# Optimization experiments

Measured on AMD Instinct MI355X. Metric: run time of the kernel, lower is better.

Reference implementation:

```python
import jax, jax.numpy as jnp
import numpy as np
import math

B, N, C = 2, 2048, 1024
H = 16
D = C // H  # 64


def setup_inputs() -> dict:
    key = jax.random.key(0)
    ks = jax.random.split(key, 11)
    s = 0.02
    return {
        "x": jax.random.normal(ks[0], (B, N, C), jnp.float32),
        "context": jax.random.normal(ks[1], (B, N, C), jnp.float32),
        "attn_bias": jax.random.normal(ks[2], (1, H, N, N), jnp.float32),
        "Wq": jax.random.normal(ks[3], (C, C), jnp.float32) * s,
        "bq": jnp.zeros((C,), jnp.float32),
        "Wk": jax.random.normal(ks[4], (C, C), jnp.float32) * s,
        "bk": jnp.zeros((C,), jnp.float32),
        "Wv": jax.random.normal(ks[5], (C, C), jnp.float32) * s,
        "bv": jnp.zeros((C,), jnp.float32),
        "Wo": jax.random.normal(ks[6], (C, C), jnp.float32) * s,
        "bo": jnp.zeros((C,), jnp.float32),
    }


def reference(x, context, attn_bias, Wq, bq, Wk, bk, Wv, bv, Wo, bo):
    scale = 1.0 / math.sqrt(D)
    # projections (torch Linear: y = x @ W.T + b), reshape to heads
    q = (x @ Wq.T + bq).reshape(B, N, H, D)
    k = (context @ Wk.T + bk).reshape(B, N, H, D)
    v = (context @ Wv.T + bv).reshape(B, N, H, D)
    # scores: (B, H, Nq, Nk)
    sim = jnp.einsum("bqhd,bkhd->bhqk", q, k) * scale + attn_bias
    attn = jax.nn.softmax(sim, axis=-1)
    o = jnp.einsum("bhqk,bkhd->bqhd", attn, v).reshape(B, N, C)
    return o @ Wo.T + bo
```

## Files before the change

### kernel.cpp

```cpp
#include <hip/hip_runtime.h>
#include <stdint.h>
#include <stddef.h>

typedef unsigned short u16;
typedef __attribute__((ext_vector_type(4))) float f32x4;
typedef __attribute__((ext_vector_type(4))) unsigned short u16x4;
typedef __attribute__((ext_vector_type(8))) __bf16 bf16x8;

#define LOG2E 1.44269504088896340736f
#define MSHIFT 23.0831169f

__device__ __forceinline__ u16 f2bf(float f){
  union { float f; uint32_t u; } a; a.f = f;
  uint32_t u = a.u;
  uint32_t r = (u + 0x7FFFu + ((u >> 16) & 1u)) >> 16;
  return (u16)r;
}

__device__ __forceinline__ void gl_lds16(const void* g, void* l){
  __builtin_amdgcn_global_load_lds(
      (const __attribute__((address_space(1))) void*)g,
      (__attribute__((address_space(3))) void*)l,
      16, 0, 0);
}

__global__ __launch_bounds__(256) void cvt6(
    const float* s0, u16* d0, int n0, float f0,
    const float* s1, u16* d1, int n1, float f1,
    const float* s2, u16* d2, int n2, float f2,
    const float* s3, u16* d3, int n3, float f3,
    const float* s4, u16* d4, int n4, float f4,
    const float* s5, u16* d5, int n5, float f5)
{
  const float* s; u16* d; int n; float f;
  switch (blockIdx.y){
    case 0: s=s0; d=d0; n=n0; f=f0; break;
    case 1: s=s1; d=d1; n=n1; f=f1; break;
    case 2: s=s2; d=d2; n=n2; f=f2; break;
    case 3: s=s3; d=d3; n=n3; f=f3; break;
    case 4: s=s4; d=d4; n=n4; f=f4; break;
    default: s=s5; d=d5; n=n5; f=f5; break;
  }
  int tid = blockIdx.x * blockDim.x + threadIdx.x;
  int stride = gridDim.x * blockDim.x;
  for (int i = tid * 4; i < n; i += stride * 4){
    f32x4 v = *(const f32x4*)(s + i);
    u16x4 o;
    o[0] = f2bf(v[0] * f); o[1] = f2bf(v[1] * f);
    o[2] = f2bf(v[2] * f); o[3] = f2bf(v[3] * f);
    *(u16x4*)(d + i) = o;
  }
}

__global__ __launch_bounds__(256, 2) void qkv_gemm(
    const u16* __restrict__ xb, const u16* __restrict__ ctxb,
    const u16* __restrict__ wq, const u16* __restrict__ wkv,
    const float* __restrict__ bq, const float* __restrict__ bk,
    const float* __restrict__ bv,
    u16* __restrict__ q_ws, u16* __restrict__ k_ws, u16* __restrict__ vt_ws)
{
  __shared__ u16 lsA[128 * 64];
  __shared__ u16 lsB[128 * 64];
  const int bid = blockIdx.x;
  const int nb = bid % 24, mb = bid / 24;
  const int tid = threadIdx.x, wave = tid >> 6, lane = tid & 63;
  const int l15 = lane & 15, lg = lane >> 4;
  const int wr = wave >> 1, wc = wave & 1;

  const u16* A; const u16* Bt; const float* bias; int outmode; int nloc;
  float bmul = 1.0f;
  if (nb < 8)      { A = xb;   Bt = wq  + (size_t)(nb * 128) * 1024;            bias = bq; bmul = 0.125f; outmode = 0; nloc = nb; }
  else if (nb < 16){ A = ctxb; Bt = wkv + (size_t)((nb - 8) * 128) * 1024;      bias = bk; outmode = 1; nloc = nb - 8; }
  else             { A = ctxb; Bt = wkv + (size_t)((1024 + (nb - 16) * 128)) * 1024; bias = bv; outmode = 2; nloc = nb - 16; }

  f32x4 acc[4][4] = {};
  const char* Ab = (const char*)(A + (size_t)(mb * 128) * 1024);
  const char* Bb = (const char*)Bt;

  for (int k0 = 0; k0 < 1024; k0 += 64){
    #pragma unroll
    for (int i = 0; i < 4; i++){
      int o = i * 4096 + wave * 1024 + lane * 16;
      int row = o >> 7, cb = o & 127;
      gl_lds16(Ab + (size_t)row * 2048 + (k0 << 1) + cb, (char*)lsA + i * 4096 + wave * 1024);
      gl_lds16(Bb + (size_t)row * 2048 + (k0 << 1) + cb, (char*)lsB + i * 4096 + wave * 1024);
    }
    __syncthreads();
    #pragma unroll
    for (int kk = 0; kk < 2; kk++){
      bf16x8 af[4], bfr[4];
      #pragma unroll
      for (int m = 0; m < 4; m++)
        af[m] = *(const bf16x8*)&lsA[(wr * 64 + m * 16 + l15) * 64 + kk * 32 + lg * 8];
      #pragma unroll
      for (int n = 0; n < 4; n++)
        bfr[n] = *(const bf16x8*)&lsB[(wc * 64 + n * 16 + l15) * 64 + kk * 32 + lg * 8];
      #pragma unroll
      for (int m = 0; m < 4; m++)
        #pragma unroll
        for (int n = 0; n < 4; n++)
          acc[m][n] = __builtin_amdgcn_mfma_f32_16x16x32_bf16(af[m], bfr[n], acc[m][n], 0, 0, 0);
    }
    __syncthreads();
  }

  #pragma unroll
  for (int n = 0; n < 4; n++){
    int colL = nloc * 128 + wc * 64 + n * 16 + l15;
    float bvv = bias[colL] * bmul;
    #pragma unroll
    for (int m = 0; m < 4; m++){
      int row0 = mb * 128 + wr * 64 + m * 16 + lg * 4;
      f32x4 v = acc[m][n];
      if (outmode == 0){
        #pragma unroll
        for (int j = 0; j < 4; j++) q_ws[(size_t)(row0 + j) * 1024 + colL] = f2bf(v[j] + bvv);
      } else if (outmode == 1){
        #pragma unroll
        for (int j = 0; j < 4; j++) k_ws[(size_t)(row0 + j) * 1024 + colL] = f2bf(v[j] + bvv);
      } else {
        int h = colL >> 6, d = colL & 63, b = row0 >> 11, tok = row0 & 2047;
        u16x4 o;
        o[0] = f2bf(v[0] + bvv); o[1] = f2bf(v[1] + bvv);
        o[2] = f2bf(v[2] + bvv); o[3] = f2bf(v[3] + bvv);
        *(u16x4*)&vt_ws[((size_t)((b * 16 + h) * 64 + d)) * 2048 + tok] = o;
      }
    }
  }
}

__global__ __launch_bounds__(256, 2) void attn(
    const u16* __restrict__ q_ws, const u16* __restrict__ k_ws,
    const u16* __restrict__ vt_ws, const float* __restrict__ bias,
    u16* __restrict__ o_ws)
{
  __shared__ u16 lsQ[128 * 64];
  __shared__ u16 lsK[2][64 * 64];
  __shared__ u16 lsV[2][64 * 64];

  const int bid = blockIdx.x;
  const int x8 = bid & 7, rr = bid >> 3;
  const int l = (((rr >> 1) * 8 + x8) << 1) | (rr & 1);
  const int b = l & 1, h = (l >> 1) & 15, qb = l >> 5;
  const int tid = threadIdx.x, wave = tid >> 6, lane = tid & 63;
  const int l15 = lane & 15, lg = lane >> 4;

  const char* Qg = (const char*)(q_ws + ((size_t)(b * 2048 + qb * 128)) * 1024 + h * 64);
  #pragma unroll
  for (int i = 0; i < 4; i++){
    int o = i * 4096 + wave * 1024 + lane * 16;
    int row = o >> 7, cb = o & 127;
    gl_lds16(Qg + (size_t)row * 2048 + cb, (char*)lsQ + i * 4096 + wave * 1024);
  }

  const char* Kg = (const char*)(k_ws + ((size_t)(b * 2048)) * 1024 + h * 64);
  const char* Vg = (const char*)(vt_ws + ((size_t)((b * 16 + h) * 64)) * 2048);

  auto stageKV = [&](int t, int buf){
    #pragma unroll
    for (int i = 0; i < 2; i++){
      int o = i * 4096 + wave * 1024 + lane * 16;
      int row = o >> 7, cb = o & 127;
      int cbs = cb ^ ((row & 7) << 4);
      gl_lds16(Kg + (size_t)(t * 64 + row) * 2048 + cbs, (char*)lsK[buf] + i * 4096 + wave * 1024);
      gl_lds16(Vg + (size_t)row * 4096 + (size_t)t * 128 + cbs, (char*)lsV[buf] + i * 4096 + wave * 1024);
    }
  };
  stageKV(0, 0);
  __syncthreads();

  bf16x8 qf[2][2];
  #pragma unroll
  for (int m = 0; m < 2; m++)
    #pragma unroll
    for (int kk = 0; kk < 2; kk++)
      qf[m][kk] = *(const bf16x8*)&lsQ[(wave * 32 + m * 16 + l15) * 64 + kk * 32 + lg * 8];

  const float* bp[2][4];
  #pragma unroll
  for (int m = 0; m < 2; m++)
    #pragma unroll
    for (int j = 0; j < 4; j++){
      int qrow = qb * 128 + wave * 32 + m * 16 + lg * 4 + j;
      bp[m][j] = bias + (size_t)h * 2048 * 2048 + (size_t)qrow * 2048 + l15;
    }

  f32x4 oacc[2][4] = {};
  float lr[2][4] = {};

  int cur = 0;
  for (int t = 0; t < 32; ++t){
    if (t + 1 < 32) stageKV(t + 1, cur ^ 1);

    float bb[2][4][4];
    #pragma unroll
    for (int m = 0; m < 2; m++)
      #pragma unroll
      for (int j = 0; j < 4; j++)
        #pragma unroll
        for (int n = 0; n < 4; n++)
          bb[m][j][n] = fmaf(bp[m][j][t * 64 + n * 16], LOG2E, -MSHIFT);

    f32x4 s[2][4] = {};
    #pragma unroll
    for (int kk = 0; kk < 2; kk++){
      bf16x8 kf[4];
      #pragma unroll
      for (int n = 0; n < 4; n++){
        int row = n * 16 + l15;
        int cbyte = (kk * 64 + lg * 16) ^ ((row & 7) << 4);
        kf[n] = *(const bf16x8*)((const char*)lsK[cur] + row * 128 + cbyte);
      }
      #pragma unroll
      for (int m = 0; m < 2; m++)
        #pragma unroll
        for (int n = 0; n < 4; n++)
          s[m][n] = __builtin_amdgcn_mfma_f32_16x16x32_bf16(qf[m][kk], kf[n], s[m][n], 0, 0, 0);
    }

    #pragma unroll
    for (int m = 0; m < 2; m++){
      #pragma unroll
      for (int j = 0; j < 4; j++){
        float p0 = __builtin_amdgcn_exp2f(fmaf(s[m][0][j], LOG2E, bb[m][j][0]));
        float p1 = __builtin_amdgcn_exp2f(fmaf(s[m][1][j], LOG2E, bb[m][j][1]));
        float p2 = __builtin_amdgcn_exp2f(fmaf(s[m][2][j], LOG2E, bb[m][j][2]));
        float p3 = __builtin_amdgcn_exp2f(fmaf(s[m][3][j], LOG2E, bb[m][j][3]));
        lr[m][j] += (p0 + p1) + (p2 + p3);
        int prow = m * 16 + lg * 4 + j;
        char* pbase = (char*)lsQ + wave * 4096 + prow * 128;
        int sw = (prow & 7) << 4;
        *(u16*)(pbase + ((  0 + l15 * 2) ^ sw)) = f2bf(p0);
        *(u16*)(pbase + (( 32 + l15 * 2) ^ sw)) = f2bf(p1);
        *(u16*)(pbase + (( 64 + l15 * 2) ^ sw)) = f2bf(p2);
        *(u16*)(pbase + (( 96 + l15 * 2) ^ sw)) = f2bf(p3);
      }
    }

    #pragma unroll
    for (int kk = 0; kk < 2; kk++){
      bf16x8 pf[2];
      #pragma unroll
      for (int m = 0; m < 2; m++){
        int prow = m * 16 + l15;
        int cbyte = (kk * 64 + lg * 16) ^ ((prow & 7) << 4);
        pf[m] = *(const bf16x8*)((const char*)lsQ + wave * 4096 + prow * 128 + cbyte);
      }
      bf16x8 vf[4];
      #pragma unroll
      for (int n = 0; n < 4; n++){
        int row = n * 16 + l15;
        int cbyte = (kk * 64 + lg * 16) ^ ((row & 7) << 4);
        vf[n] = *(const bf16x8*)((const char*)lsV[cur] + row * 128 + cbyte);
      }
      #pragma unroll
      for (int m = 0; m < 2; m++)
        #pragma unroll
        for (int n = 0; n < 4; n++)
          oacc[m][n] = __builtin_amdgcn_mfma_f32_16x16x32_bf16(pf[m], vf[n], oacc[m][n], 0, 0, 0);
    }

    __syncthreads();
    cur ^= 1;
  }

  #pragma unroll
  for (int m = 0; m < 2; m++)
    #pragma unroll
    for (int j = 0; j < 4; j++){
      float rs = lr[m][j];
      rs += __shfl_xor(rs, 1); rs += __shfl_xor(rs, 2);
      rs += __shfl_xor(rs, 4); rs += __shfl_xor(rs, 8);
      float inv = 1.0f / rs;
      int tok = b * 2048 + qb * 128 + wave * 32 + m * 16 + lg * 4 + j;
      #pragma unroll
      for (int n = 0; n < 4; n++)
        o_ws[(size_t)tok * 1024 + h * 64 + n * 16 + l15] = f2bf(oacc[m][n][j] * inv);
    }
}

__global__ __launch_bounds__(256, 2) void out_gemm(
    const u16* __restrict__ o_ws, const u16* __restrict__ wo,
    const float* __restrict__ bo, float* __restrict__ out)
{
  __shared__ u16 lsA[128 * 64];
  __shared__ u16 lsB[128 * 64];
  const int bid = blockIdx.x;
  const int nb = bid % 8, mb = bid / 8;
  const int tid = threadIdx.x, wave = tid >> 6, lane = tid & 63;
  const int l15 = lane & 15, lg = lane >> 4;
  const int wr = wave >> 1, wc = wave & 1;

  f32x4 acc[4][4] = {};
  const char* Ab = (const char*)(o_ws + (size_t)(mb * 128) * 1024);
  const char* Bb = (const char*)(wo + (size_t)(nb * 128) * 1024);

  for (int k0 = 0; k0 < 1024; k0 += 64){
    #pragma unroll
    for (int i = 0; i < 4; i++){
      int o = i * 4096 + wave * 1024 + lane * 16;
      int row = o >> 7, cb = o & 127;
      gl_lds16(Ab + (size_t)row * 2048 + (k0 << 1) + cb, (char*)lsA + i * 4096 + wave * 1024);
      gl_lds16(Bb + (size_t)row * 2048 + (k0 << 1) + cb, (char*)lsB + i * 4096 + wave * 1024);
    }
    __syncthreads();
    #pragma unroll
    for (int kk = 0; kk < 2; kk++){
      bf16x8 af[4], bfr[4];
      #pragma unroll
      for (int m = 0; m < 4; m++)
        af[m] = *(const bf16x8*)&lsA[(wr * 64 + m * 16 + l15) * 64 + kk * 32 + lg * 8];
      #pragma unroll
      for (int n = 0; n < 4; n++)
        bfr[n] = *(const bf16x8*)&lsB[(wc * 64 + n * 16 + l15) * 64 + kk * 32 + lg * 8];
      #pragma unroll
      for (int m = 0; m < 4; m++)
        #pragma unroll
        for (int n = 0; n < 4; n++)
          acc[m][n] = __builtin_amdgcn_mfma_f32_16x16x32_bf16(af[m], bfr[n], acc[m][n], 0, 0, 0);
    }
    __syncthreads();
  }

  #pragma unroll
  for (int n = 0; n < 4; n++){
    int col = nb * 128 + wc * 64 + n * 16 + l15;
    float bvv = bo[col];
    #pragma unroll
    for (int m = 0; m < 4; m++){
      int row0 = mb * 128 + wr * 64 + m * 16 + lg * 4;
      f32x4 v = acc[m][n];
      #pragma unroll
      for (int j = 0; j < 4; j++)
        out[(size_t)(row0 + j) * 1024 + col] = v[j] + bvv;
    }
  }
}

extern "C" void kernel_launch(void* const* d_in, const int* in_sizes, int n_in,
                              void* d_out, int out_size, void* d_ws, size_t ws_size,
                              hipStream_t stream)
{
  const float* x    = (const float*)d_in[0];
  const float* ctx  = (const float*)d_in[1];
  const float* bias = (const float*)d_in[2];
  const float* Wq   = (const float*)d_in[3];
  const float* bq   = (const float*)d_in[4];
  const float* Wk   = (const float*)d_in[5];
  const float* bk   = (const float*)d_in[6];
  const float* Wv   = (const float*)d_in[7];
  const float* bv   = (const float*)d_in[8];
  const float* Wo   = (const float*)d_in[9];
  const float* bo   = (const float*)d_in[10];
  float* out = (float*)d_out;

  char* ws = (char*)d_ws;
  u16* xb    = (u16*)(ws);
  u16* ctxb  = (u16*)(ws +  8388608);
  u16* wq_b  = (u16*)(ws + 16777216);
  u16* wkv_b = (u16*)(ws + 18874368);
  u16* wo_b  = (u16*)(ws + 23068672);
  u16* q_ws  = (u16*)(ws + 25165824);
  u16* k_ws  = (u16*)(ws + 33554432);
  u16* vt_ws = (u16*)(ws + 41943040);
  u16* o_ws  = xb;

  cvt6<<<dim3(1024, 6), 256, 0, stream>>>(
      x,   xb,    4194304, 1.0f,
      ctx, ctxb,  4194304, 1.0f,
      Wq,  wq_b,  1048576, 0.125f,
      Wk,  wkv_b, 1048576, 1.0f,
      Wv,  wkv_b + 1048576, 1048576, 1.0f,
      Wo,  wo_b,  1048576, 1.0f);

  qkv_gemm<<<768, 256, 0, stream>>>(xb, ctxb, wq_b, wkv_b, bq, bk, bv, q_ws, k_ws, vt_ws);
  attn<<<512, 256, 0, stream>>>(q_ws, k_ws, vt_ws, bias, o_ws);
  out_gemm<<<256, 256, 0, stream>>>(o_ws, wo_b, bo, out);
}
```

Measured before the change: 551.5 us.

## Halve attention and out-GEMM tiles, raise occupancy, prefetch bias one tile ahead

After: 2.053 ms. +272.2%, slower.

```diff
diff --git a/kernel.cpp b/kernel.cpp
--- a/kernel.cpp
+++ b/kernel.cpp
@@ -129,12 +129,12 @@
   }
 }
 
-__global__ __launch_bounds__(256, 2) void attn(
+__global__ __launch_bounds__(256, 4) void attn(
     const u16* __restrict__ q_ws, const u16* __restrict__ k_ws,
     const u16* __restrict__ vt_ws, const float* __restrict__ bias,
     u16* __restrict__ o_ws)
 {
-  __shared__ u16 lsQ[128 * 64];
+  __shared__ u16 lsQ[64 * 64];
   __shared__ u16 lsK[2][64 * 64];
   __shared__ u16 lsV[2][64 * 64];
 
@@ -145,12 +145,12 @@
   const int tid = threadIdx.x, wave = tid >> 6, lane = tid & 63;
   const int l15 = lane & 15, lg = lane >> 4;
 
-  const char* Qg = (const char*)(q_ws + ((size_t)(b * 2048 + qb * 128)) * 1024 + h * 64);
-  #pragma unroll
-  for (int i = 0; i < 4; i++){
+  const char* Qg = (const char*)(q_ws + ((size_t)(b * 2048 + qb * 64)) * 1024 + h * 64);
+  #pragma unroll
+  for (int i = 0; i < 2; i++){
     int o = i * 4096 + wave * 1024 + lane * 16;
     int row = o >> 7, cb = o & 127;
-    gl_lds16(Qg + (size_t)row * 2048 + cb, (char*)lsQ + i * 4096 + wave * 1024);
+    gl_lds16(Qg + (size_t)row * 2048 + cb, (char*)lsQ + o);
   }
 
   const char* Kg = (const char*)(k_ws + ((size_t)(b * 2048)) * 1024 + h * 64);
@@ -162,46 +162,40 @@
       int o = i * 4096 + wave * 1024 + lane * 16;
       int row = o >> 7, cb = o & 127;
       int cbs = cb ^ ((row & 7) << 4);
-      gl_lds16(Kg + (size_t)(t * 64 + row) * 2048 + cbs, (char*)lsK[buf] + i * 4096 + wave * 1024);
-      gl_lds16(Vg + (size_t)row * 4096 + (size_t)t * 128 + cbs, (char*)lsV[buf] + i * 4096 + wave * 1024);
+      gl_lds16(Kg + (size_t)(t * 64 + row) * 2048 + cbs, (char*)lsK[buf] + o);
+      gl_lds16(Vg + (size_t)row * 4096 + (size_t)t * 128 + cbs, (char*)lsV[buf] + o);
     }
   };
+
+  const float* bp[4];
+  #pragma unroll
+  for (int j = 0; j < 4; j++){
+    int qrow = qb * 64 + wave * 16 + lg * 4 + j;
+    bp[j] = bias + (size_t)h * 4194304 + (size_t)qrow * 2048 + l15;
+  }
+  float bbA[4][4], bbB[4][4];
+  auto loadbias = [&](float (&bb)[4][4], int t){
+    #pragma unroll
+    for (int j = 0; j < 4; j++)
+      #pragma unroll
+      for (int n = 0; n < 4; n++)
+        bb[j][n] = bp[j][t * 64 + n * 16];
+  };
+
   stageKV(0, 0);
+  loadbias(bbA, 0);
   __syncthreads();
 
-  bf16x8 qf[2][2];
-  #pragma unroll
-  for (int m = 0; m < 2; m++)
-    #pragma unroll
-    for (int kk = 0; kk < 2; kk++)
-      qf[m][kk] = *(const bf16x8*)&lsQ[(wave * 32 + m * 16 + l15) * 64 + kk * 32 + lg * 8];
-
-  const float* bp[2][4];
-  #pragma unroll
-  for (int m = 0; m < 2; m++)
-    #pragma unroll
-    for (int j = 0; j < 4; j++){
-      int qrow = qb * 128 + wave * 32 + m * 16 + lg * 4 + j;
-      bp[m][j] = bias + (size_t)h * 2048 * 2048 + (size_t)qrow * 2048 + l15;
-    }
-
-  f32x4 oacc[2][4] = {};
-  float lr[2][4] = {};
-
-  int cur = 0;
-  for (int t = 0; t < 32; ++t){
-    if (t + 1 < 32) stageKV(t + 1, cur ^ 1);
-
-    float bb[2][4][4];
-    #pragma unroll
-    for (int m = 0; m < 2; m++)
-      #pragma unroll
-      for (int j = 0; j < 4; j++)
-        #pragma unroll
-        for (int n = 0; n < 4; n++)
-          bb[m][j][n] = fmaf(bp[m][j][t * 64 + n * 16], LOG2E, -MSHIFT);
-
-    f32x4 s[2][4] = {};
+  bf16x8 qf[2];
+  #pragma unroll
+  for (int kk = 0; kk < 2; kk++)
+    qf[kk] = *(const bf16x8*)&lsQ[(wave * 16 + l15) * 64 + kk * 32 + lg * 8];
+
+  f32x4 oacc[4] = {};
+  float lr[4] = {};
+
+  auto body = [&](int t, int buf, float (&bb)[4][4]){
+    f32x4 s[4] = {};
     #pragma unroll
     for (int kk = 0; kk < 2; kk++){
       bf16x8 kf[4];
@@ -209,114 +203,110 @@
       for (int n = 0; n < 4; n++){
         int row = n * 16 + l15;
         int cbyte = (kk * 64 + lg * 16) ^ ((row & 7) << 4);
-        kf[n] = *(const bf16x8*)((const char*)lsK[cur] + row * 128 + cbyte);
+        kf[n] = *(const bf16x8*)((const char*)lsK[buf] + row * 128 + cbyte);
       }
+      #pragma unroll
+      for (int n = 0; n < 4; n++)
+        s[n] = __builtin_amdgcn_mfma_f32_16x16x32_bf16(qf[kk], kf[n], s[n], 0, 0, 0);
+    }
+    #pragma unroll
+    for (int j = 0; j < 4; j++){
+      float p0 = __builtin_amdgcn_exp2f(fmaf(s[0][j] + bb[j][0], LOG2E, -MSHIFT));
+      float p1 = __builtin_amdgcn_exp2f(fmaf(s[1][j] + bb[j][1], LOG2E, -MSHIFT));
+      float p2 = __builtin_amdgcn_exp2f(fmaf(s[2][j] + bb[j][2], LOG2E, -MSHIFT));
+      float p3 = __builtin_amdgcn_exp2f(fmaf(s[3][j] + bb[j][3], LOG2E, -MSHIFT));
+      lr[j] += (p0 + p1) + (p2 + p3);
+      int prow = lg * 4 + j;
+      char* pbase = (char*)lsQ + wave * 2048 + prow * 128;
+      int sw = (prow & 7) << 4;
+      *(u16*)(pbase + ((  0 + l15 * 2) ^ sw)) = f2bf(p0);
+      *(u16*)(pbase + (( 32 + l15 * 2) ^ sw)) = f2bf(p1);
+      *(u16*)(pbase + (( 64 + l15 * 2) ^ sw)) = f2bf(p2);
+      *(u16*)(pbase + (( 96 + l15 * 2) ^ sw)) = f2bf(p3);
+    }
+    #pragma unroll
+    for (int kk = 0; kk < 2; kk++){
+      int cb_p = (kk * 64 + lg * 16) ^ ((l15 & 7) << 4);
+      bf16x8 pf = *(const bf16x8*)((const char*)lsQ + wave * 2048 + l15 * 128 + cb_p);
+      bf16x8 vf[4];
+      #pragma unroll
+      for (int n = 0; n < 4; n++){
+        int row = n * 16 + l15;
+        int cbyte = (kk * 64 + lg * 16) ^ ((row & 7) << 4);
+        vf[n] = *(const bf16x8*)((const char*)lsV[buf] + row * 128 + cbyte);
+      }
+      #pragma unroll
+      for (int n = 0; n < 4; n++)
+        oacc[n] = __builtin_amdgcn_mfma_f32_16x16x32_bf16(pf, vf[n], oacc[n], 0, 0, 0);
+    }
+  };
+
+  for (int t = 0; t < 32; t += 2){
+    stageKV(t + 1, 1);
+    loadbias(bbB, t + 1);
+    body(t, 0, bbA);
+    __syncthreads();
+    if (t + 2 < 32){ stageKV(t + 2, 0); loadbias(bbA, t + 2); }
+    body(t + 1, 1, bbB);
+    __syncthreads();
+  }
+
+  #pragma unroll
+  for (int j = 0; j < 4; j++){
+    float rs = lr[j];
+    rs += __shfl_xor(rs, 1); rs += __shfl_xor(rs, 2);
+    rs += __shfl_xor(rs, 4); rs += __shfl_xor(rs, 8);
+    float inv = 1.0f / rs;
+    int tok = b * 2048 + qb * 64 + wave * 16 + lg * 4 + j;
+    #pragma unroll
+    for (int n = 0; n < 4; n++)
+      o_ws[(size_t)tok * 1024 + h * 64 + n * 16 + l15] = f2bf(oacc[n][j] * inv);
+  }
+}
+
+__global__ __launch_bounds__(256, 2) void out_gemm(
+    const u16* __restrict__ o_ws, const u16* __restrict__ wo,
+    const float* __restrict__ bo, float* __restrict__ out)
+{
+  __shared__ u16 lsA[64 * 64];
+  __shared__ u16 lsB[128 * 64];
+  const int bid = blockIdx.x;
+  const int nb = bid & 7, mb = bid >> 3;
+  const int tid = threadIdx.x, wave = tid >> 6, lane = tid & 63;
+  const int l15 = lane & 15, lg = lane >> 4;
+  const int wr = wave >> 1, wc = wave & 1;
+
+  f32x4 acc[2][4] = {};
+  const char* Ab = (const char*)(o_ws + (size_t)(mb * 64) * 1024);
+  const char* Bb = (const char*)(wo + (size_t)(nb * 128) * 1024);
+
+  for (int k0 = 0; k0 < 1024; k0 += 64){
+    #pragma unroll
+    for (int i = 0; i < 2; i++){
+      int o = i * 4096 + wave * 1024 + lane * 16;
+      int row = o >> 7, cb = o & 127;
+      gl_lds16(Ab + (size_t)row * 2048 + (k0 << 1) + cb, (char*)lsA + o);
+    }
+    #pragma unroll
+    for (int i = 0; i < 4; i++){
+      int o = i * 4096 + wave * 1024 + lane * 16;
+      int row = o >> 7, cb = o & 127;
+      gl_lds16(Bb + (size_t)row * 2048 + (k0 << 1) + cb, (char*)lsB + o);
+    }
+    __syncthreads();
+    #pragma unroll
+    for (int kk = 0; kk < 2; kk++){
+      bf16x8 af[2], bfr[4];
+      #pragma unroll
+      for (int m = 0; m < 2; m++)
+        af[m] = *(const bf16x8*)&lsA[(wr * 32 + m * 16 + l15) * 64 + kk * 32 + lg * 8];
+      #pragma unroll
+      for (int n = 0; n < 4; n++)
+        bfr[n] = *(const bf16x8*)&lsB[(wc * 64 + n * 16 + l15) * 64 + kk * 32 + lg * 8];
       #pragma unroll
       for (int m = 0; m < 2; m++)
         #pragma unroll
         for (int n = 0; n < 4; n++)
-          s[m][n] = __builtin_amdgcn_mfma_f32_16x16x32_bf16(qf[m][kk], kf[n], s[m][n], 0, 0, 0);
-    }
-
-    #pragma unroll
-    for (int m = 0; m < 2; m++){
-      #pragma unroll
-      for (int j = 0; j < 4; j++){
-        float p0 = __builtin_amdgcn_exp2f(fmaf(s[m][0][j], LOG2E, bb[m][j][0]));
-        float p1 = __builtin_amdgcn_exp2f(fmaf(s[m][1][j], LOG2E, bb[m][j][1]));
-        float p2 = __builtin_amdgcn_exp2f(fmaf(s[m][2][j], LOG2E, bb[m][j][2]));
-        float p3 = __builtin_amdgcn_exp2f(fmaf(s[m][3][j], LOG2E, bb[m][j][3]));
-        lr[m][j] += (p0 + p1) + (p2 + p3);
-        int prow = m * 16 + lg * 4 + j;
-        char* pbase = (char*)lsQ + wave * 4096 + prow * 128;
-        int sw = (prow & 7) << 4;
-        *(u16*)(pbase + ((  0 + l15 * 2) ^ sw)) = f2bf(p0);
-        *(u16*)(pbase + (( 32 + l15 * 2) ^ sw)) = f2bf(p1);
-        *(u16*)(pbase + (( 64 + l15 * 2) ^ sw)) = f2bf(p2);
-        *(u16*)(pbase + (( 96 + l15 * 2) ^ sw)) = f2bf(p3);
-      }
-    }
-
-    #pragma unroll
-    for (int kk = 0; kk < 2; kk++){
-      bf16x8 pf[2];
-      #pragma unroll
-      for (int m = 0; m < 2; m++){
-        int prow = m * 16 + l15;
-        int cbyte = (kk * 64 + lg * 16) ^ ((prow & 7) << 4);
-        pf[m] = *(const bf16x8*)((const char*)lsQ + wave * 4096 + prow * 128 + cbyte);
-      }
-      bf16x8 vf[4];
-      #pragma unroll
-      for (int n = 0; n < 4; n++){
-        int row = n * 16 + l15;
-        int cbyte = (kk * 64 + lg * 16) ^ ((row & 7) << 4);
-        vf[n] = *(const bf16x8*)((const char*)lsV[cur] + row * 128 + cbyte);
-      }
-      #pragma unroll
-      for (int m = 0; m < 2; m++)
-        #pragma unroll
-        for (int n = 0; n < 4; n++)
-          oacc[m][n] = __builtin_amdgcn_mfma_f32_16x16x32_bf16(pf[m], vf[n], oacc[m][n], 0, 0, 0);
-    }
-
-    __syncthreads();
-    cur ^= 1;
-  }
-
-  #pragma unroll
-  for (int m = 0; m < 2; m++)
-    #pragma unroll
-    for (int j = 0; j < 4; j++){
-      float rs = lr[m][j];
-      rs += __shfl_xor(rs, 1); rs += __shfl_xor(rs, 2);
-      rs += __shfl_xor(rs, 4); rs += __shfl_xor(rs, 8);
-      float inv = 1.0f / rs;
-      int tok = b * 2048 + qb * 128 + wave * 32 + m * 16 + lg * 4 + j;
-      #pragma unroll
-      for (int n = 0; n < 4; n++)
-        o_ws[(size_t)tok * 1024 + h * 64 + n * 16 + l15] = f2bf(oacc[m][n][j] * inv);
-    }
-}
-
-__global__ __launch_bounds__(256, 2) void out_gemm(
-    const u16* __restrict__ o_ws, const u16* __restrict__ wo,
-    const float* __restrict__ bo, float* __restrict__ out)
-{
-  __shared__ u16 lsA[128 * 64];
-  __shared__ u16 lsB[128 * 64];
-  const int bid = blockIdx.x;
-  const int nb = bid % 8, mb = bid / 8;
-  const int tid = threadIdx.x, wave = tid >> 6, lane = tid & 63;
-  const int l15 = lane & 15, lg = lane >> 4;
-  const int wr = wave >> 1, wc = wave & 1;
-
-  f32x4 acc[4][4] = {};
-  const char* Ab = (const char*)(o_ws + (size_t)(mb * 128) * 1024);
-  const char* Bb = (const char*)(wo + (size_t)(nb * 128) * 1024);
-
-  for (int k0 = 0; k0 < 1024; k0 += 64){
-    #pragma unroll
-    for (int i = 0; i < 4; i++){
-      int o = i * 4096 + wave * 1024 + lane * 16;
-      int row = o >> 7, cb = o & 127;
-      gl_lds16(Ab + (size_t)row * 2048 + (k0 << 1) + cb, (char*)lsA + i * 4096 + wave * 1024);
-      gl_lds16(Bb + (size_t)row * 2048 + (k0 << 1) + cb, (char*)lsB + i * 4096 + wave * 1024);
-    }
-    __syncthreads();
-    #pragma unroll
-    for (int kk = 0; kk < 2; kk++){
-      bf16x8 af[4], bfr[4];
-      #pragma unroll
-      for (int m = 0; m < 4; m++)
-        af[m] = *(const bf16x8*)&lsA[(wr * 64 + m * 16 + l15) * 64 + kk * 32 + lg * 8];
-      #pragma unroll
-      for (int n = 0; n < 4; n++)
-        bfr[n] = *(const bf16x8*)&lsB[(wc * 64 + n * 16 + l15) * 64 + kk * 32 + lg * 8];
-      #pragma unroll
-      for (int m = 0; m < 4; m++)
-        #pragma unroll
-        for (int n = 0; n < 4; n++)
           acc[m][n] = __builtin_amdgcn_mfma_f32_16x16x32_bf16(af[m], bfr[n], acc[m][n], 0, 0, 0);
     }
     __syncthreads();
@@ -327,8 +317,8 @@
     int col = nb * 128 + wc * 64 + n * 16 + l15;
     float bvv = bo[col];
     #pragma unroll
-    for (int m = 0; m < 4; m++){
-      int row0 = mb * 128 + wr * 64 + m * 16 + lg * 4;
+    for (int m = 0; m < 2; m++){
+      int row0 = mb * 64 + wr * 32 + m * 16 + lg * 4;
       f32x4 v = acc[m][n];
       #pragma unroll
       for (int j = 0; j < 4; j++)
@@ -374,6 +364,6 @@
       Wo,  wo_b,  1048576, 1.0f);
 
   qkv_gemm<<<768, 256, 0, stream>>>(xb, ctxb, wq_b, wkv_b, bq, bk, bv, q_ws, k_ws, vt_ws);
-  attn<<<512, 256, 0, stream>>>(q_ws, k_ws, vt_ws, bias, o_ws);
-  out_gemm<<<256, 256, 0, stream>>>(o_ws, wo_b, bo, out);
-}
+  attn<<<1024, 256, 0, stream>>>(q_ws, k_ws, vt_ws, bias, o_ws);
+  out_gemm<<<512, 256, 0, stream>>>(o_ws, wo_b, bo, out);
+}
```
